# Performance work log

Measured on AMD Instinct MI355X. Metric: run time of the kernel, lower is better.

Reference implementation:

```python
import jax, jax.numpy as jnp
import numpy as np

NEG_SLOPE = 0.2  # DGL GATConv/GATv2Conv default negative_slope


def _seg_softmax(score, dst, N):
    # softmax over incoming edges per destination node; score: (E, H)
    m = jax.ops.segment_max(score, dst, num_segments=N)          # (N, H)
    ex = jnp.exp(score - m[dst])
    s = jax.ops.segment_sum(ex, dst, num_segments=N)             # (N, H)
    return ex / s[dst]


def _gatv2(h, src, dst, Ws, Wd, attn, bias, N):
    # GATv2: e_ij = a^T LeakyReLU(W_s h_src + W_d h_dst)
    H, D = attn.shape
    fs = (h @ Ws).reshape(N, H, D)
    fd = (h @ Wd).reshape(N, H, D)
    e = jax.nn.leaky_relu(fs[src] + fd[dst], NEG_SLOPE)          # (E, H, D)
    score = jnp.einsum('ehd,hd->eh', e, attn)                    # (E, H)
    alpha = _seg_softmax(score, dst, N)
    out = jax.ops.segment_sum(fs[src] * alpha[:, :, None], dst, num_segments=N)
    return out + bias.reshape(1, H, D)                           # (N, H, D)


def _gat(h, src, dst, W, al, ar, bias, N):
    # GAT v1: e_ij = LeakyReLU(a_l . W h_src + a_r . W h_dst)
    H, D = al.shape
    f = (h @ W).reshape(N, H, D)
    el = jnp.einsum('nhd,hd->nh', f, al)
    er = jnp.einsum('nhd,hd->nh', f, ar)
    score = jax.nn.leaky_relu(el[src] + er[dst], NEG_SLOPE)      # (E, H)
    alpha = _seg_softmax(score, dst, N)
    out = jax.ops.segment_sum(f[src] * alpha[:, :, None], dst, num_segments=N)
    return out + bias.reshape(1, H, D)                           # (N, H, D)


def setup_inputs() -> dict:
    key = jax.random.key(0)
    N, E, V, ED = 50000, 800000, 32, 128   # nodes, edges, node types, embed_dim
    H, D = 4, 32                           # heads, per-head dim (hidden = 128)
    ks = jax.random.split(key, 20)
    rn = lambda k, shp, s: jax.random.normal(k, shp, dtype=jnp.float32) * s
    hid = H * D
    return {
        'in_feat': jax.random.randint(ks[0], (N,), 0, V),
        'src': jax.random.randint(ks[1], (E,), 0, N),
        'dst': jax.random.randint(ks[2], (E,), 0, N),
        'emb': rn(ks[3], (V, ED), 0.02),
        'W1s': rn(ks[4], (ED, hid), 1.0 / np.sqrt(ED)),
        'W1d': rn(ks[5], (ED, hid), 1.0 / np.sqrt(ED)),
        'a1': rn(ks[6], (H, D), 1.0 / np.sqrt(D)),
        'b1': jnp.zeros((hid,), jnp.float32),
        'W2s': rn(ks[7], (hid, hid), 1.0 / np.sqrt(hid)),
        'W2d': rn(ks[8], (hid, hid), 1.0 / np.sqrt(hid)),
        'a2': rn(ks[9], (H, D), 1.0 / np.sqrt(D)),
        'b2': jnp.zeros((hid,), jnp.float32),
        'Wc': rn(ks[10], (hid, H * V), 1.0 / np.sqrt(hid)),
        'al': rn(ks[11], (H, V), 1.0 / np.sqrt(V)),
        'ar': rn(ks[12], (H, V), 1.0 / np.sqrt(V)),
        'bc': jnp.zeros((H * V,), jnp.float32),
    }


def reference(in_feat, src, dst, emb, W1s, W1d, a1, b1, W2s, W2d, a2, b2, Wc, al, ar, bc):
    N = in_feat.shape[0]
    h = emb[in_feat]                                              # (N, 128)
    h = jax.nn.elu(_gatv2(h, src, dst, W1s, W1d, a1, b1, N).reshape(N, -1))
    h = jax.nn.elu(_gatv2(h, src, dst, W2s, W2d, a2, b2, N).reshape(N, -1))
    h = _gat(h, src, dst, Wc, al, ar, bc, N)                      # (N, H, V)
    return jax.nn.softmax(h.mean(axis=1), axis=-1)                # (N, V)
```

## Files before the change

kernel.cpp:

```cpp
#include <hip/hip_runtime.h>
#include <hip/hip_bf16.h>

typedef unsigned short u16;
typedef unsigned int u32;

typedef __bf16 bf16x8 __attribute__((ext_vector_type(8)));
typedef float f32x4 __attribute__((ext_vector_type(4)));

#define NEG_SLOPE 0.2f
#define CAP 5120

__device__ __forceinline__ float bf2f(u16 u){
  union { u32 i; float f; } c; c.i = ((u32)u) << 16; return c.f;
}
__device__ __forceinline__ u16 f2bf(float f){
  __hip_bfloat16 h = __float2bfloat16(f);
  u16 u; __builtin_memcpy(&u, &h, 2); return u;
}
__device__ __forceinline__ u32 pack2(float a, float b){
  return (u32)f2bf(a) | ((u32)f2bf(b) << 16);
}
__device__ __forceinline__ float2 bfpair(u32 v){
  union { u32 i; float f; } a, b;
  a.i = v << 16; b.i = v & 0xffff0000u;
  return make_float2(a.f, b.f);
}
__device__ __forceinline__ float lrelu(float x){
  return fmaxf(x, 0.f) + NEG_SLOPE * fminf(x, 0.f);
}
__device__ __forceinline__ float eluf(float x){
  return x > 0.f ? x : (__expf(x) - 1.f);
}
__device__ __forceinline__ bf16x8 ld_frag(const uint4* p){
  uint4 u = *p;
  bf16x8 r;
  __builtin_memcpy(&r, &u, 16);
  return r;
}

__global__ void k_probe(const u16* __restrict__ w, int* __restrict__ flag){
  int t = threadIdx.x;
  int hit = 0;
  for (int i = t; i < 4096; i += 64){
    u16 v = w[i];
    int e = (v >> 7) & 0xFF;
    if (e >= 200) hit = 1;
  }
  unsigned long long b = __ballot(hit);
  if (t == 0) flag[0] = b ? 1 : 0;
}

struct Params13 {
  const void* src[13];
  int off[13];
  int n[13];
};

__global__ void k_cvt(Params13 P, const int* __restrict__ flag, float* __restrict__ dst){
  int t = blockIdx.y;
  int i = blockIdx.x*256 + threadIdx.x;
  if (i >= P.n[t]) return;
  int f = flag[0];
  float v = f ? ((const float*)P.src[t])[i] : bf2f(((const u16*)P.src[t])[i]);
  dst[P.off[t] + i] = v;
}

__global__ void k_wprep(const float* __restrict__ pr, u16* __restrict__ wp){
  int g = blockIdx.x*256 + threadIdx.x;
  if (g >= 3*16384) return;
  int m = g >> 14;
  int e = g & 16383;
  int j    = e & 7;
  int lane = (e >> 3) & 63;
  int kb   = (e >> 9) & 3;
  int nt   = (e >> 11) & 7;
  int k = kb*32 + (lane >> 4)*8 + j;
  int n = nt*16 + (lane & 15);
  const int Woff[3] = {37120, 53504, 70144};
  wp[g] = f2bf(pr[Woff[m] + k*128 + n]);
}

__global__ __launch_bounds__(256) void k_bin(
    const int* __restrict__ src, const int* __restrict__ dst, const int* __restrict__ vf,
    int* __restrict__ gcnt, u32* __restrict__ bbuf, int E){
  __shared__ int lcnt[256];
  __shared__ int lloc[256];
  int t = threadIdx.x;
  lcnt[t] = 0;
  __syncthreads();
  int base = blockIdx.x*2048;
  int s[8], d[8];
  #pragma unroll
  for (int k=0;k<8;++k){
    int i = base + k*256 + t;
    if (i < E){ s[k]=src[i]; d[k]=dst[i]; atomicAdd(&lcnt[d[k]>>8], 1); }
    else s[k] = -1;
  }
  __syncthreads();
  if (lcnt[t] > 0) lloc[t] = atomicAdd(&gcnt[t], lcnt[t]);
  __syncthreads();
  #pragma unroll
  for (int k=0;k<8;++k){
    if (s[k] >= 0){
      int b = d[k]>>8;
      int pos = atomicAdd(&lloc[b], 1);
      if (pos < CAP)
        bbuf[(size_t)b*CAP + pos] = ((u32)s[k]<<13) | ((u32)vf[s[k]]<<8) | (u32)(d[k]&255);
    }
  }
}

__global__ __launch_bounds__(256) void k_bcnt(
    const u32* __restrict__ bbuf, const int* __restrict__ gcnt,
    u32* __restrict__ H, int* __restrict__ deg, int N){
  __shared__ u32 lh[8192];
  __shared__ int ldeg[256];
  int b = blockIdx.x;
  int t = threadIdx.x;
  for (int i=t;i<8192;i+=256) lh[i]=0;
  ldeg[t]=0;
  __syncthreads();
  int n = gcnt[b]; if (n > CAP) n = CAP;
  const u32* bb = bbuf + (size_t)b*CAP;
  for (int i=t;i<n;i+=256){
    u32 it = bb[i];
    int ld = it & 255, v = (it>>8)&31;
    atomicAdd(&lh[ld*32+v], 1u);
    atomicAdd(&ldeg[ld], 1);
  }
  __syncthreads();
  int node0 = b*256;
  for (int i=t;i<8192;i+=256){
    int ld = i>>5;
    if (node0+ld < N) H[(size_t)(node0+ld)*32 + (i&31)] = lh[i];
  }
  if (node0+t < N) deg[node0+t] = ldeg[t];
}

__global__ __launch_bounds__(256) void k_csort(
    const u32* __restrict__ bbuf, const int* __restrict__ gcnt,
    const int* __restrict__ rowptr, int* __restrict__ esrc, int N){
  __shared__ int cur[256];
  int b = blockIdx.x;
  int t = threadIdx.x;
  int node0 = b*256;
  cur[t] = (node0+t < N) ? rowptr[node0+t] : 0;
  __syncthreads();
  int n = gcnt[b]; if (n > CAP) n = CAP;
  const u32* bb = bbuf + (size_t)b*CAP;
  for (int i=t;i<n;i+=256){
    u32 it = bb[i];
    int ld = it & 255;
    int pos = atomicAdd(&cur[ld], 1);
    esrc[pos] = (int)(it >> 13);
  }
}

__global__ __launch_bounds__(256) void k_bsum(const int* __restrict__ deg,
                                              int* __restrict__ bsum, int N){
  __shared__ int ws[4];
  int t = threadIdx.x;
  int i = blockIdx.x*256 + t;
  int v = (i < N) ? deg[i] : 0;
  #pragma unroll
  for (int off=32; off>=1; off>>=1) v += __shfl_down(v, off);
  if ((t & 63) == 0) ws[t>>6] = v;
  __syncthreads();
  if (t == 0) bsum[blockIdx.x] = ws[0]+ws[1]+ws[2]+ws[3];
}

__global__ void k_scanb(const int* __restrict__ bsum, int* __restrict__ boff,
                        int* __restrict__ rowptr, int nb, int N){
  int l = threadIdx.x;
  int carry = 0;
  int nChunk = (nb + 63) >> 6;
  for (int c = 0; c < nChunk; ++c){
    int idx = (c << 6) + l;
    int v = (idx < nb) ? bsum[idx] : 0;
    int x = v;
    #pragma unroll
    for (int off=1; off<64; off<<=1){
      int y = __shfl_up(x, off);
      if (l >= off) x += y;
    }
    if (idx < nb) boff[idx] = carry + x - v;
    carry += __shfl(x, 63);
  }
  if (l == 0) rowptr[N] = carry;
}

__global__ __launch_bounds__(256) void k_scan2(const int* __restrict__ deg,
                                               const int* __restrict__ boff,
                                               int* __restrict__ rowptr, int N){
  __shared__ int ws[4];
  int t = threadIdx.x;
  int i = blockIdx.x*256 + t;
  int lane = t & 63, wid = t >> 6;
  int v = (i < N) ? deg[i] : 0;
  int x = v;
  #pragma unroll
  for (int off=1; off<64; off<<=1){
    int y = __shfl_up(x, off);
    if (lane >= off) x += y;
  }
  if (lane == 63) ws[wid] = x;
  __syncthreads();
  int woff = 0;
  #pragma unroll
  for (int w=0; w<4; ++w) woff += (w < wid) ? ws[w] : 0;
  int excl = boff[blockIdx.x] + woff + x - v;
  if (i < N) rowptr[i] = excl;
}

__global__ void k_tinyA(const float* __restrict__ pr,
                        float* __restrict__ Ts, float* __restrict__ Td){
  const float* emb = pr + 0;
  const float* W1s = pr + 4096;
  const float* W1d = pr + 20480;
  int g = blockIdx.x*256 + threadIdx.x;
  int v = g >> 7, j = g & 127;
  float as = 0.f, ad = 0.f;
  for (int k = 0; k < 128; ++k){
    float e = emb[v*128 + k];
    as += e * W1s[k*128 + j];
    ad += e * W1d[k*128 + j];
  }
  Ts[g] = as; Td[g] = ad;
}

__global__ void k_tinyB(const float* __restrict__ Ts, const float* __restrict__ Td,
                        const float* __restrict__ pr, float* __restrict__ S1){
  const float* a1 = pr + 36864;
  int g = blockIdx.x*256 + threadIdx.x;
  int vd = g >> 7, vs = (g >> 2) & 31, h = g & 3;
  float acc = 0.f;
  for (int dd = 0; dd < 32; ++dd){
    float x = Ts[vs*128 + h*32 + dd] + Td[vd*128 + h*32 + dd];
    acc += a1[h*32 + dd] * lrelu(x);
  }
  S1[g] = acc;
}

__global__ void k_tinyC(const float* __restrict__ S1, float* __restrict__ Ee){
  int g = blockIdx.x*256 + threadIdx.x;
  int vd = g >> 7, h = g & 3;
  float M = -INFINITY;
  #pragma unroll 8
  for (int vs = 0; vs < 32; ++vs) M = fmaxf(M, S1[vd*128 + vs*4 + h]);
  Ee[g] = __expf(S1[g] - M);
}

__global__ __launch_bounds__(256) void k_node1h(
    const u32* __restrict__ H, const int* __restrict__ vf,
    const float* __restrict__ Ts, const float* __restrict__ Ee,
    const float* __restrict__ pr, u32* __restrict__ hOutB, int N){
  const float* b1 = pr + 36992;
  __shared__ float TsL[4096];
  __shared__ float EL[4096];
  __shared__ float wbuf[4][32][4];
  int t = threadIdx.x;
  for (int i = t; i < 4096; i += 256){ TsL[i] = Ts[i]; EL[i] = Ee[i]; }
  __syncthreads();
  int wid = t >> 6, lane = t & 63;
  int h = lane >> 4;
  float bx = b1[lane*2], by = b1[lane*2+1];
  int base = blockIdx.x * 32;
  for (int dd = wid; dd < 32; dd += 4){
    int d = base + dd;
    if (d >= N) break;
    int tt = vf[d];
    float4 w4 = make_float4(0.f,0.f,0.f,0.f);
    if (lane < 32){
      float cf = (float)H[(size_t)d*32 + lane];
      const float4 e4 = *reinterpret_cast<const float4*>(&EL[tt*128 + lane*4]);
      w4.x = cf*e4.x; w4.y = cf*e4.y; w4.z = cf*e4.z; w4.w = cf*e4.w;
    }
    float4 sv = w4;
    #pragma unroll
    for (int off=1; off<32; off<<=1){
      sv.x += __shfl_xor(sv.x, off);
      sv.y += __shfl_xor(sv.y, off);
      sv.z += __shfl_xor(sv.z, off);
      sv.w += __shfl_xor(sv.w, off);
    }
    float sh = (h==0)?sv.x:(h==1)?sv.y:(h==2)?sv.z:sv.w;
    sh += __shfl_xor(sh, 32);
    if (lane < 32) *reinterpret_cast<float4*>(&wbuf[wid][lane][0]) = w4;
    __builtin_amdgcn_wave_barrier();
    float inv = (sh > 0.f) ? 1.f/sh : 0.f;
    float ax = 0.f, ay = 0.f;
    #pragma unroll 8
    for (int v=0; v<32; ++v){
      float wv = wbuf[wid][v][h];
      const float2 f = *reinterpret_cast<const float2*>(&TsL[v*128 + lane*2]);
      ax += wv * f.x; ay += wv * f.y;
    }
    hOutB[(size_t)d*64 + lane] = pack2(eluf(ax*inv + bx), eluf(ay*inv + by));
  }
}

template<bool TWO>
__global__ __launch_bounds__(256) void k_mfma(
    const u32* __restrict__ Xb, const u16* __restrict__ wpS, const u16* __restrict__ wpD,
    u16* __restrict__ outS, u16* __restrict__ outD, int N){
  int t = threadIdx.x;
  int w = t >> 6, l = t & 63;
  int row0 = blockIdx.x*64 + w*16;
  int ar = row0 + (l & 15);
  int ko = l >> 4;
  const uint4* Xq = reinterpret_cast<const uint4*>(Xb);
  bf16x8 a[4];
  #pragma unroll
  for (int kb=0;kb<4;++kb){
    if (ar < N) a[kb] = ld_frag(&Xq[(size_t)ar*16 + kb*4 + ko]);
    else { uint4 z = make_uint4(0,0,0,0); __builtin_memcpy(&a[kb], &z, 16); }
  }
  const uint4* WS = reinterpret_cast<const uint4*>(wpS);
  const uint4* WD = reinterpret_cast<const uint4*>(wpD);
  int col0 = l & 15;
  int rbase = row0 + (l>>4)*4;
  #pragma unroll
  for (int nt=0; nt<8; ++nt){
    f32x4 accS = {0.f,0.f,0.f,0.f};
    f32x4 accD = {0.f,0.f,0.f,0.f};
    #pragma unroll
    for (int kb=0;kb<4;++kb){
      bf16x8 bS = ld_frag(&WS[(nt*4 + kb)*64 + l]);
      accS = __builtin_amdgcn_mfma_f32_16x16x32_bf16(a[kb], bS, accS, 0,0,0);
      if (TWO){
        bf16x8 bD = ld_frag(&WD[(nt*4 + kb)*64 + l]);
        accD = __builtin_amdgcn_mfma_f32_16x16x32_bf16(a[kb], bD, accD, 0,0,0);
      }
    }
    int col = nt*16 + col0;
    #pragma unroll
    for (int r=0;r<4;++r){
      int rr = rbase + r;
      if (rr < N){
        outS[(size_t)rr*128 + col] = f2bf(accS[r]);
        if (TWO) outD[(size_t)rr*128 + col] = f2bf(accD[r]);
      }
    }
  }
}

#define UNPACK8(pv, fv)                                              \
  { float2 _p0 = bfpair(pv.x), _p1 = bfpair(pv.y),                   \
           _p2 = bfpair(pv.z), _p3 = bfpair(pv.w);                   \
    fv[0]=_p0.x; fv[1]=_p0.y; fv[2]=_p1.x; fv[3]=_p1.y;              \
    fv[4]=_p2.x; fv[5]=_p2.y; fv[6]=_p3.x; fv[7]=_p3.y; }

__global__ __launch_bounds__(256) void k_node2f(
    const int* __restrict__ rowptr, const int* __restrict__ esrc,
    const u32* __restrict__ fsb, const u32* __restrict__ fdb,
    const float* __restrict__ pr, u32* __restrict__ hOutB, int N){
  const float* a2 = pr + 69888;
  const float* b2 = pr + 70016;
  int t = threadIdx.x;
  int wid = t >> 6, lane = t & 63;
  int q = lane & 15, g = lane >> 4;
  int d = blockIdx.x*4 + wid;
  if (d >= N) return;
  int r0 = rowptr[d], r1 = rowptr[d+1];
  const uint4* fs4 = reinterpret_cast<const uint4*>(fsb);
  float a2r[8], fdr[8];
  {
    float4 t0 = *reinterpret_cast<const float4*>(a2 + q*8);
    float4 t1 = *reinterpret_cast<const float4*>(a2 + q*8 + 4);
    a2r[0]=t0.x; a2r[1]=t0.y; a2r[2]=t0.z; a2r[3]=t0.w;
    a2r[4]=t1.x; a2r[5]=t1.y; a2r[6]=t1.z; a2r[7]=t1.w;
    uint4 pv = reinterpret_cast<const uint4*>(fdb)[(size_t)d*16 + q];
    UNPACK8(pv, fdr);
  }
  float m = -INFINITY, ssum = 0.f;
  float acc[8] = {0.f,0.f,0.f,0.f,0.f,0.f,0.f,0.f};
  int i = r0 + g;
  for (; i + 4 < r1; i += 8){
    int s1 = esrc[i], s2 = esrc[i+4];
    uint4 pv1 = fs4[(size_t)s1*16 + q];
    uint4 pv2 = fs4[(size_t)s2*16 + q];
    float f1[8], f2[8];
    UNPACK8(pv1, f1);
    UNPACK8(pv2, f2);
    float p1a = 0.f, p1b = 0.f, p2a = 0.f, p2b = 0.f;
    #pragma unroll
    for (int k=0;k<8;++k){
      float x1 = f1[k] + fdr[k];
      float x2 = f2[k] + fdr[k];
      p1a = fmaf(a2r[k], x1, p1a);
      p1b = fmaf(a2r[k], fabsf(x1), p1b);
      p2a = fmaf(a2r[k], x2, p2a);
      p2b = fmaf(a2r[k], fabsf(x2), p2b);
    }
    float p1 = fmaf(0.6f, p1a, 0.4f*p1b);
    float p2 = fmaf(0.6f, p2a, 0.4f*p2b);
    p1 += __shfl_xor(p1, 1); p1 += __shfl_xor(p1, 2);
    p2 += __shfl_xor(p2, 1); p2 += __shfl_xor(p2, 2);
    float mn = fmaxf(m, fmaxf(p1, p2));
    float cor = __expf(m - mn);
    float w1 = __expf(p1 - mn);
    float w2 = __expf(p2 - mn);
    ssum = ssum*cor + w1 + w2;
    #pragma unroll
    for (int k=0;k<8;++k) acc[k] = fmaf(acc[k], cor, fmaf(w1, f1[k], w2*f2[k]));
    m = mn;
  }
  for (; i < r1; i += 4){
    int s = esrc[i];
    uint4 pv = fs4[(size_t)s*16 + q];
    float fv[8];
    UNPACK8(pv, fv);
    float pa = 0.f, pb = 0.f;
    #pragma unroll
    for (int k=0;k<8;++k){
      float x = fv[k] + fdr[k];
      pa = fmaf(a2r[k], x, pa);
      pb = fmaf(a2r[k], fabsf(x), pb);
    }
    float p = fmaf(0.6f, pa, 0.4f*pb);
    p += __shfl_xor(p, 1); p += __shfl_xor(p, 2);
    float mn = fmaxf(m, p);
    float cor = __expf(m - mn);
    float w = __expf(p - mn);
    ssum = ssum*cor + w;
    #pragma unroll
    for (int k=0;k<8;++k) acc[k] = fmaf(acc[k], cor, w*fv[k]);
    m = mn;
  }
  #pragma unroll
  for (int off = 16; off <= 32; off <<= 1){
    float mo  = __shfl_xor(m, off);
    float sso = __shfl_xor(ssum, off);
    float ao[8];
    #pragma unroll
    for (int k=0;k<8;++k) ao[k] = __shfl_xor(acc[k], off);
    float mn = fmaxf(m, mo);
    float c1 = (m  > -1e30f) ? __expf(m  - mn) : 0.f;
    float c2 = (mo > -1e30f) ? __expf(mo - mn) : 0.f;
    ssum = ssum*c1 + sso*c2;
    #pragma unroll
    for (int k=0;k<8;++k) acc[k] = acc[k]*c1 + ao[k]*c2;
    m = mn;
  }
  if (g == 0){
    float inv = (ssum > 0.f) ? 1.f/ssum : 0.f;
    float v0 = eluf(acc[0]*inv + b2[q*8+0]), v1 = eluf(acc[1]*inv + b2[q*8+1]);
    float v2 = eluf(acc[2]*inv + b2[q*8+2]), v3 = eluf(acc[3]*inv + b2[q*8+3]);
    float v4 = eluf(acc[4]*inv + b2[q*8+4]), v5 = eluf(acc[5]*inv + b2[q*8+5]);
    float v6 = eluf(acc[6]*inv + b2[q*8+6]), v7 = eluf(acc[7]*inv + b2[q*8+7]);
    uint4 ov;
    ov.x = pack2(v0,v1); ov.y = pack2(v2,v3);
    ov.z = pack2(v4,v5); ov.w = pack2(v6,v7);
    *reinterpret_cast<uint4*>(hOutB + (size_t)d*64 + q*4) = ov;
  }
}

__global__ __launch_bounds__(256) void k_node3f(
    const int* __restrict__ rowptr, const int* __restrict__ esrc,
    const float* __restrict__ el, const float* __restrict__ er, const u32* __restrict__ fb,
    const float* __restrict__ pr, const int* __restrict__ flag,
    void* __restrict__ out, int N){
  const float* bc = pr + 86784;
  int t = threadIdx.x;
  int wid = t >> 6, lane = t & 63;
  int q = lane & 15, g = lane >> 4;
  int h = q >> 2;
  int d = blockIdx.x*4 + wid;
  if (d >= N) return;
  int r0 = rowptr[d], r1 = rowptr[d+1];
  const uint4* f4g = reinterpret_cast<const uint4*>(fb);
  float erh = er[(size_t)d*4 + h];
  float m = -INFINITY, ssum = 0.f;
  float acc[8] = {0.f,0.f,0.f,0.f,0.f,0.f,0.f,0.f};
  int i = r0 + g;
  for (; i + 4 < r1; i += 8){
    int s1 = esrc[i], s2 = esrc[i+4];
    float sc1 = lrelu(el[(size_t)s1*4 + h] + erh);
    float sc2 = lrelu(el[(size_t)s2*4 + h] + erh);
    uint4 pv1 = f4g[(size_t)s1*16 + q];
    uint4 pv2 = f4g[(size_t)s2*16 + q];
    float f1[8], f2[8];
    UNPACK8(pv1, f1);
    UNPACK8(pv2, f2);
    float mn = fmaxf(m, fmaxf(sc1, sc2));
    float cor = __expf(m - mn);
    float w1 = __expf(sc1 - mn);
    float w2 = __expf(sc2 - mn);
    ssum = ssum*cor + w1 + w2;
    #pragma unroll
    for (int k=0;k<8;++k) acc[k] = fmaf(acc[k], cor, fmaf(w1, f1[k], w2*f2[k]));
    m = mn;
  }
  for (; i < r1; i += 4){
    int s = esrc[i];
    float sc = lrelu(el[(size_t)s*4 + h] + erh);
    uint4 pv = f4g[(size_t)s*16 + q];
    float fv[8];
    UNPACK8(pv, fv);
    float mn = fmaxf(m, sc);
    float cor = __expf(m - mn);
    float w = __expf(sc - mn);
    ssum = ssum*cor + w;
    #pragma unroll
    for (int k=0;k<8;++k) acc[k] = fmaf(acc[k], cor, w*fv[k]);
    m = mn;
  }
  #pragma unroll
  for (int off = 16; off <= 32; off <<= 1){
    float mo  = __shfl_xor(m, off);
    float sso = __shfl_xor(ssum, off);
    float ao[8];
    #pragma unroll
    for (int k=0;k<8;++k) ao[k] = __shfl_xor(acc[k], off);
    float mn = fmaxf(m, mo);
    float c1 = (m  > -1e30f) ? __expf(m  - mn) : 0.f;
    float c2 = (mo > -1e30f) ? __expf(mo - mn) : 0.f;
    ssum = ssum*c1 + sso*c2;
    #pragma unroll
    for (int k=0;k<8;++k) acc[k] = acc[k]*c1 + ao[k]*c2;
    m = mn;
  }
  float inv = (ssum > 0.f) ? 1.f/ssum : 0.f;
  float v[8];
  #pragma unroll
  for (int k=0;k<8;++k) v[k] = acc[k]*inv + bc[q*8+k];
  #pragma unroll
  for (int k=0;k<8;++k){
    v[k] += __shfl_xor(v[k], 4);
    v[k] += __shfl_xor(v[k], 8);
    v[k] *= 0.25f;
  }
  float mm = fmaxf(fmaxf(fmaxf(v[0],v[1]),fmaxf(v[2],v[3])),
                   fmaxf(fmaxf(v[4],v[5]),fmaxf(v[6],v[7])));
  mm = fmaxf(mm, __shfl_xor(mm, 1));
  mm = fmaxf(mm, __shfl_xor(mm, 2));
  float ex[8]; float se = 0.f;
  #pragma unroll
  for (int k=0;k<8;++k){ ex[k] = __expf(v[k]-mm); se += ex[k]; }
  se += __shfl_xor(se, 1);
  se += __shfl_xor(se, 2);
  float rs = 1.f/se;
  if (lane < 4){
    if (flag[0]){
      float4 o0 = make_float4(ex[0]*rs, ex[1]*rs, ex[2]*rs, ex[3]*rs);
      float4 o1 = make_float4(ex[4]*rs, ex[5]*rs, ex[6]*rs, ex[7]*rs);
      *reinterpret_cast<float4*>((float*)out + (size_t)d*32 + q*8)     = o0;
      *reinterpret_cast<float4*>((float*)out + (size_t)d*32 + q*8 + 4) = o1;
    } else {
      u32* o = (u32*)out + (size_t)d*16 + q*4;
      o[0] = pack2(ex[0]*rs, ex[1]*rs);
      o[1] = pack2(ex[2]*rs, ex[3]*rs);
      o[2] = pack2(ex[4]*rs, ex[5]*rs);
      o[3] = pack2(ex[6]*rs, ex[7]*rs);
    }
  }
}

__global__ void k_el(const u32* __restrict__ fb, const float* __restrict__ pr,
                     float* __restrict__ el, float* __restrict__ er, int N){
  const float* al = pr + 86528;
  const float* ar = pr + 86656;
  int g = blockIdx.x*256 + threadIdx.x;
  if (g >= N*4) return;
  int n = g >> 2, h = g & 3;
  const uint4* f4 = reinterpret_cast<const uint4*>(fb) + (size_t)n*16 + h*4;
  float aL=0.f, aR=0.f;
  #pragma unroll
  for (int q=0;q<4;++q){
    uint4 pv = f4[q];
    float fv[8];
    UNPACK8(pv, fv);
    const float* alp = al + h*32 + q*8;
    const float* arp = ar + h*32 + q*8;
    #pragma unroll
    for (int k=0;k<8;++k){
      aL += alp[k]*fv[k];
      aR += arp[k]*fv[k];
    }
  }
  el[g] = aL; er[g] = aR;
}

extern "C" void kernel_launch(void* const* d_in, const int* in_sizes, int n_in,
                              void* d_out, int out_size, void* d_ws, size_t ws_size,
                              hipStream_t stream){
  const int* in_feat = (const int*)d_in[0];
  const int* src     = (const int*)d_in[1];
  const int* dstA    = (const int*)d_in[2];
  const int N = in_sizes[0];
  const int E = in_sizes[1];

  char* p = (char*)d_ws;
  auto alloc = [&](size_t bytes)->char*{
    char* r = p; p += (bytes + 255) & ~(size_t)255; return r;
  };
  float* big0   = (float*)alloc((size_t)N*128*4);
  float* big1   = (float*)alloc((size_t)N*128*4);
  float* big2   = (float*)alloc((size_t)N*128*4);
  int*   deg    = (int*)alloc((size_t)N*4);
  int*   rowptr = (int*)alloc((size_t)(N+1)*4);
  int*   bsum   = (int*)alloc(1024*4);
  int*   boff   = (int*)alloc(1024*4);
  int*   esrc   = (int*)alloc((size_t)E*4);
  int*   gcnt   = (int*)alloc(256*4);
  float* Ts     = (float*)alloc(4096*4);
  float* Td     = (float*)alloc(4096*4);
  float* S1     = (float*)alloc(4096*4);
  float* Ee     = (float*)alloc(4096*4);
  float* el     = (float*)alloc((size_t)N*4*4);
  float* er     = (float*)alloc((size_t)N*4*4);
  float* parena = (float*)alloc(86912*4);
  u16*   wpack  = (u16*)alloc(3*16384*2);
  int*   flag   = (int*)alloc(256);

  u32* H    = (u32*)big0;
  u32* bbuf = (u32*)big1;

  k_probe<<<1,64,0,stream>>>((const u16*)d_in[4], flag);
  Params13 P;
  const int sz[13]  = {4096,16384,16384,128,128,16384,16384,128,128,16384,128,128,128};
  int off = 0;
  for (int t = 0; t < 13; ++t){
    P.src[t] = d_in[3 + t];
    P.n[t] = sz[t];
    P.off[t] = off;
    off += sz[t];
  }
  k_cvt<<<dim3(64,13),256,0,stream>>>(P, flag, parena);
  k_wprep<<<192,256,0,stream>>>(parena, wpack);

  int nbkt = (N + 255)/256;
  hipMemsetAsync(gcnt, 0, 256*4, stream);
  int gBin = (E + 2047)/2048;
  k_bin<<<gBin,256,0,stream>>>(src, dstA, in_feat, gcnt, bbuf, E);
  k_bcnt<<<nbkt,256,0,stream>>>(bbuf, gcnt, H, deg, N);
  int nb = (N + 255)/256;
  k_bsum<<<nb,256,0,stream>>>(deg, bsum, N);
  k_scanb<<<1,64,0,stream>>>(bsum, boff, rowptr, nb, N);
  k_scan2<<<nb,256,0,stream>>>(deg, boff, rowptr, N);
  k_csort<<<nbkt,256,0,stream>>>(bbuf, gcnt, rowptr, esrc, N);

  k_tinyA<<<16,256,0,stream>>>(parena, Ts, Td);
  k_tinyB<<<16,256,0,stream>>>(Ts, Td, parena, S1);
  k_tinyC<<<16,256,0,stream>>>(S1, Ee);

  u32* h1b = (u32*)big2;
  int gN32 = (N + 31)/32;
  k_node1h<<<gN32,256,0,stream>>>(H, in_feat, Ts, Ee, parena, h1b, N);

  int gG = (N + 63)/64;
  u16* fs2b = (u16*)big0;
  u16* fd2b = (u16*)big1;
  k_mfma<true><<<gG,256,0,stream>>>(h1b, wpack, wpack + 16384, fs2b, fd2b, N);

  int gN4 = (N + 3)/4;
  u32* h2b = (u32*)big2;
  k_node2f<<<gN4,256,0,stream>>>(rowptr, esrc, (u32*)fs2b, (u32*)fd2b, parena, h2b, N);

  u16* f3b = (u16*)big0;
  k_mfma<false><<<gG,256,0,stream>>>(h2b, wpack + 32768, nullptr, f3b, nullptr, N);

  int gEl = (int)(((size_t)N*4 + 255)/256);
  k_el<<<gEl,256,0,stream>>>((u32*)f3b, parena, el, er, N);

  k_node3f<<<gN4,256,0,stream>>>(rowptr, esrc, el, er, (u32*)f3b, parena, flag, d_out, N);
}
```

Before: 236.2 us.

## Split layer-1 aggregation into weight computation plus MFMA matmul with block-diagonal Ts

Layer-1 output per node is a weighted sum over the 32 source node types of the Ts rows. The node kernel now only computes the normalized per-(type, head) attention weights and writes them in bf16. A new MFMA kernel multiplies those weights by a block-diagonal packed Ts matrix and applies bias plus ELU. This removes the per-node scalar FMA loop and the large shared-memory staging of Ts and Ee per block. The cost is an extra kernel launch, an extra N x 128 bf16 round trip through global memory, and bf16 rounding of the weights.

```diff
diff --git a/kernel.cpp b/kernel.cpp
--- a/kernel.cpp
+++ b/kernel.cpp
@@ -80,6 +80,19 @@
   wp[g] = f2bf(pr[Woff[m] + k*128 + n]);
 }
 
+__global__ void k_t1prep(const float* __restrict__ Ts, u16* __restrict__ tp){
+  int g = blockIdx.x*256 + threadIdx.x;
+  if (g >= 16384) return;
+  int j    = g & 7;
+  int lane = (g >> 3) & 63;
+  int kb   = (g >> 9) & 3;
+  int nt   = (g >> 11) & 7;
+  int k = kb*32 + (lane >> 4)*8 + j;
+  int n = nt*16 + (lane & 15);
+  int h = k >> 5, hp = n >> 5, v = k & 31;
+  tp[g] = (h == hp) ? f2bf(Ts[v*128 + n]) : (u16)0;
+}
+
 __global__ __launch_bounds__(256) void k_bin(
     const int* __restrict__ src, const int* __restrict__ dst, const int* __restrict__ vf,
     int* __restrict__ gcnt, u32* __restrict__ bbuf, int E){
@@ -250,20 +263,11 @@
   Ee[g] = __expf(S1[g] - M);
 }
 
-__global__ __launch_bounds__(256) void k_node1h(
+__global__ __launch_bounds__(256) void k_node1w(
     const u32* __restrict__ H, const int* __restrict__ vf,
-    const float* __restrict__ Ts, const float* __restrict__ Ee,
-    const float* __restrict__ pr, u32* __restrict__ hOutB, int N){
-  const float* b1 = pr + 36992;
-  __shared__ float TsL[4096];
-  __shared__ float EL[4096];
-  __shared__ float wbuf[4][32][4];
-  int t = threadIdx.x;
-  for (int i = t; i < 4096; i += 256){ TsL[i] = Ts[i]; EL[i] = Ee[i]; }
-  __syncthreads();
+    const float* __restrict__ Ee, u16* __restrict__ wnb, int N){
+  int t = threadIdx.x;
   int wid = t >> 6, lane = t & 63;
-  int h = lane >> 4;
-  float bx = b1[lane*2], by = b1[lane*2+1];
   int base = blockIdx.x * 32;
   for (int dd = wid; dd < 32; dd += 4){
     int d = base + dd;
@@ -272,7 +276,7 @@
     float4 w4 = make_float4(0.f,0.f,0.f,0.f);
     if (lane < 32){
       float cf = (float)H[(size_t)d*32 + lane];
-      const float4 e4 = *reinterpret_cast<const float4*>(&EL[tt*128 + lane*4]);
+      const float4 e4 = *reinterpret_cast<const float4*>(Ee + tt*128 + lane*4);
       w4.x = cf*e4.x; w4.y = cf*e4.y; w4.z = cf*e4.z; w4.w = cf*e4.w;
     }
     float4 sv = w4;
@@ -283,19 +287,17 @@
       sv.z += __shfl_xor(sv.z, off);
       sv.w += __shfl_xor(sv.w, off);
     }
-    float sh = (h==0)?sv.x:(h==1)?sv.y:(h==2)?sv.z:sv.w;
-    sh += __shfl_xor(sh, 32);
-    if (lane < 32) *reinterpret_cast<float4*>(&wbuf[wid][lane][0]) = w4;
-    __builtin_amdgcn_wave_barrier();
-    float inv = (sh > 0.f) ? 1.f/sh : 0.f;
-    float ax = 0.f, ay = 0.f;
-    #pragma unroll 8
-    for (int v=0; v<32; ++v){
-      float wv = wbuf[wid][v][h];
-      const float2 f = *reinterpret_cast<const float2*>(&TsL[v*128 + lane*2]);
-      ax += wv * f.x; ay += wv * f.y;
-    }
-    hOutB[(size_t)d*64 + lane] = pack2(eluf(ax*inv + bx), eluf(ay*inv + by));
+    if (lane < 32){
+      float ix = (sv.x > 0.f) ? 1.f/sv.x : 0.f;
+      float iy = (sv.y > 0.f) ? 1.f/sv.y : 0.f;
+      float iz = (sv.z > 0.f) ? 1.f/sv.z : 0.f;
+      float iw = (sv.w > 0.f) ? 1.f/sv.w : 0.f;
+      u16* row = wnb + (size_t)d*128;
+      row[      lane] = f2bf(w4.x*ix);
+      row[ 32 + lane] = f2bf(w4.y*iy);
+      row[ 64 + lane] = f2bf(w4.z*iz);
+      row[ 96 + lane] = f2bf(w4.w*iw);
+    }
   }
 }
 
@@ -340,6 +342,43 @@
         outS[(size_t)rr*128 + col] = f2bf(accS[r]);
         if (TWO) outD[(size_t)rr*128 + col] = f2bf(accD[r]);
       }
+    }
+  }
+}
+
+__global__ __launch_bounds__(256) void k_mfma1(
+    const u32* __restrict__ Xb, const u16* __restrict__ tp, const float* __restrict__ pr,
+    u16* __restrict__ outB, int N){
+  const float* b1 = pr + 36992;
+  int t = threadIdx.x;
+  int w = t >> 6, l = t & 63;
+  int row0 = blockIdx.x*64 + w*16;
+  int ar = row0 + (l & 15);
+  int ko = l >> 4;
+  const uint4* Xq = reinterpret_cast<const uint4*>(Xb);
+  bf16x8 a[4];
+  #pragma unroll
+  for (int kb=0;kb<4;++kb){
+    if (ar < N) a[kb] = ld_frag(&Xq[(size_t)ar*16 + kb*4 + ko]);
+    else { uint4 z = make_uint4(0,0,0,0); __builtin_memcpy(&a[kb], &z, 16); }
+  }
+  const uint4* WB = reinterpret_cast<const uint4*>(tp);
+  int col0 = l & 15;
+  int rbase = row0 + (l>>4)*4;
+  #pragma unroll
+  for (int nt=0; nt<8; ++nt){
+    f32x4 acc = {0.f,0.f,0.f,0.f};
+    #pragma unroll
+    for (int kb=0;kb<4;++kb){
+      bf16x8 b = ld_frag(&WB[(nt*4 + kb)*64 + l]);
+      acc = __builtin_amdgcn_mfma_f32_16x16x32_bf16(a[kb], b, acc, 0,0,0);
+    }
+    int col = nt*16 + col0;
+    float bv = b1[col];
+    #pragma unroll
+    for (int r=0;r<4;++r){
+      int rr = rbase + r;
+      if (rr < N) outB[(size_t)rr*128 + col] = f2bf(eluf(acc[r] + bv));
     }
   }
 }
@@ -610,11 +649,12 @@
   float* el     = (float*)alloc((size_t)N*4*4);
   float* er     = (float*)alloc((size_t)N*4*4);
   float* parena = (float*)alloc(86912*4);
-  u16*   wpack  = (u16*)alloc(3*16384*2);
+  u16*   wpack  = (u16*)alloc(4*16384*2);
   int*   flag   = (int*)alloc(256);
 
   u32* H    = (u32*)big0;
   u32* bbuf = (u32*)big1;
+  u16* tpack = wpack + 3*16384;
 
   k_probe<<<1,64,0,stream>>>((const u16*)d_in[4], flag);
   Params13 P;
@@ -643,15 +683,18 @@
   k_tinyA<<<16,256,0,stream>>>(parena, Ts, Td);
   k_tinyB<<<16,256,0,stream>>>(Ts, Td, parena, S1);
   k_tinyC<<<16,256,0,stream>>>(S1, Ee);
-
-  u32* h1b = (u32*)big2;
+  k_t1prep<<<64,256,0,stream>>>(Ts, tpack);
+
+  u16* h1b = (u16*)big2;
+  u16* wnb = (u16*)big2 + (size_t)N*128;
   int gN32 = (N + 31)/32;
-  k_node1h<<<gN32,256,0,stream>>>(H, in_feat, Ts, Ee, parena, h1b, N);
-
+  k_node1w<<<gN32,256,0,stream>>>(H, in_feat, Ee, wnb, N);
   int gG = (N + 63)/64;
+  k_mfma1<<<gG,256,0,stream>>>((u32*)wnb, tpack, parena, h1b, N);
+
   u16* fs2b = (u16*)big0;
   u16* fd2b = (u16*)big1;
-  k_mfma<true><<<gG,256,0,stream>>>(h1b, wpack, wpack + 16384, fs2b, fd2b, N);
+  k_mfma<true><<<gG,256,0,stream>>>((u32*)h1b, wpack, wpack + 16384, fs2b, fd2b, N);
 
   int gN4 = (N + 3)/4;
   u32* h2b = (u32*)big2;
```

Measured after the change: 231.5 us, median of 2. 2.0% less time.
